# Optimization experiments

Measured on AMD Instinct MI355X. Metric: run time of the kernel, lower is better.

## Reference

```python
import jax, jax.numpy as jnp
import numpy as np

N_NODES = 50000
N_EDGES = 400000
IN_DIM = 64
HID = 128
HEADS = 4
NEG_SLOPE = 0.2


def gat_conv(x, src, dst, W, a_src, a_dst, b, heads, out_ch, concat):
    N = x.shape[0]
    h = (x @ W).reshape(N, heads, out_ch)                 # [N,H,C]
    alpha_s = jnp.einsum('nhc,hc->nh', h, a_src)          # [N,H]
    alpha_d = jnp.einsum('nhc,hc->nh', h, a_dst)
    e = jax.nn.leaky_relu(alpha_s[src] + alpha_d[dst], NEG_SLOPE)  # [E,H]
    m = jax.ops.segment_max(e, dst, num_segments=N)
    m = jnp.where(jnp.isfinite(m), m, 0.0)
    ex = jnp.exp(e - m[dst])
    s = jax.ops.segment_sum(ex, dst, num_segments=N)
    alpha = ex / s[dst]                                   # segment softmax over incoming edges
    out = jax.ops.segment_sum(h[src] * alpha[:, :, None], dst, num_segments=N)  # [N,H,C]
    out = out.reshape(N, heads * out_ch) if concat else out.mean(axis=1)
    return out + b


def setup_inputs() -> dict:
    key = jax.random.key(0)
    ks = jax.random.split(key, 20)
    g = lambda i, shape, sc: (jax.random.normal(ks[i], shape, jnp.float32) * sc)
    x = g(0, (N_NODES, IN_DIM), 1.0)
    edge_index = jax.random.randint(ks[1], (2, N_EDGES), 0, N_NODES, dtype=jnp.int32)
    d = {
        'x': x, 'edge_index': edge_index,
        'W1': g(2, (IN_DIM, HEADS * HID), 0.1), 'a_src1': g(3, (HEADS, HID), 0.1), 'a_dst1': g(4, (HEADS, HID), 0.1), 'b1': jnp.zeros((HEADS * HID,), jnp.float32),
        'W2': g(5, (HEADS * HID, HEADS * HID), 0.05), 'a_src2': g(6, (HEADS, HID), 0.1), 'a_dst2': g(7, (HEADS, HID), 0.1), 'b2': jnp.zeros((HEADS * HID,), jnp.float32),
        'W3': g(8, (HEADS * HID, HID), 0.05), 'a_src3': g(9, (1, HID), 0.1), 'a_dst3': g(10, (1, HID), 0.1), 'b3': jnp.zeros((HID,), jnp.float32),
        'fc1_w': g(11, (HID, HID // 2), 0.1), 'fc1_b': jnp.zeros((HID // 2,), jnp.float32),
        'fc2_w': g(12, (HID // 2, 1), 0.1), 'fc2_b': jnp.zeros((1,), jnp.float32),
    }
    return d


def reference(x, edge_index, W1, a_src1, a_dst1, b1, W2, a_src2, a_dst2, b2, W3, a_src3, a_dst3, b3, fc1_w, fc1_b, fc2_w, fc2_b):
    N = x.shape[0]
    loop = jnp.arange(N, dtype=edge_index.dtype)
    src = jnp.concatenate([edge_index[0], loop])  # PyG GATConv adds self-loops by default
    dst = jnp.concatenate([edge_index[1], loop])
    h = jax.nn.elu(gat_conv(x, src, dst, W1, a_src1, a_dst1, b1, HEADS, HID, True))
    h = jax.nn.elu(gat_conv(h, src, dst, W2, a_src2, a_dst2, b2, HEADS, HID, True))
    h = jax.nn.elu(gat_conv(h, src, dst, W3, a_src3, a_dst3, b3, 1, HID, False))
    h = jax.nn.relu(h @ fc1_w + fc1_b)
    return jax.nn.sigmoid(h @ fc2_w + fc2_b)  # [N, 1]
```

## Files before the change

### kernel.cpp

```cpp
#include <hip/hip_runtime.h>
#include <math.h>

typedef __attribute__((ext_vector_type(8))) short short8;
typedef __attribute__((ext_vector_type(4))) float f32x4;
typedef unsigned short u16;
typedef unsigned int u32;

__device__ inline u16 f2b(float f) {
  u32 u = __float_as_uint(f);
  return (u16)((u + 0x7FFFu + ((u >> 16) & 1u)) >> 16);
}
__device__ inline float b2f(u16 b) { return __uint_as_float((u32)b << 16); }
__device__ inline float lrelu(float v) { return v > 0.f ? v : 0.2f * v; }
__device__ inline float elu1(float v) { return v > 0.f ? v : __expf(v) - 1.f; }

__device__ inline void gld_lds16(const void* g, void* l) {
  __builtin_amdgcn_global_load_lds((const __attribute__((address_space(1))) void*)g,
                                   (__attribute__((address_space(3))) void*)l, 16, 0, 0);
}

__global__ void fused_prep(const float* __restrict__ W1, u16* __restrict__ Wt1,
                           const float* __restrict__ W2, u16* __restrict__ Wt2,
                           const float* __restrict__ W3, u16* __restrict__ Wt3,
                           const int* __restrict__ ei, int E0, int ET,
                           int* __restrict__ deg) {
  int i = blockIdx.x * blockDim.x + threadIdx.x;
  if (i < 64 * 512) {
    int k = i / 512, n = i % 512;
    Wt1[n * 64 + k] = f2b(W1[i]);
    return;
  }
  i -= 64 * 512;
  if (i < 512 * 512) {
    int k = i / 512, n = i % 512;
    Wt2[n * 512 + k] = f2b(W2[i]);
    return;
  }
  i -= 512 * 512;
  if (i < 512 * 128) {
    int k = i / 128, n = i % 128;
    Wt3[n * 512 + k] = f2b(W3[i]);
    return;
  }
  i -= 512 * 128;
  if (i < ET) {
    int d = (i < E0) ? ei[E0 + i] : (i - E0);
    atomicAdd(&deg[d], 1);
  }
}

__global__ __launch_bounds__(256) void gemm_bf16_gat(
    const u16* __restrict__ A, const u16* __restrict__ Bt, u16* __restrict__ Hb,
    const float* __restrict__ a_src, const float* __restrict__ a_dst,
    float* __restrict__ aS, float* __restrict__ aD, int M, int HC, int K, int Hh,
    int gy, int nStrips) {
  int mIdx, nIdx;
  if (nStrips == 4) {
    int l = blockIdx.x;
    int xcd = l & 7, k = l >> 3;
    nIdx = k & 3;
    mIdx = xcd + 8 * (k >> 2);
    if (mIdx >= gy) return;
  } else {
    mIdx = blockIdx.x;
    nIdx = 0;
  }
  __shared__ u16 As[2][128 * 32];
  __shared__ u16 Bs[2][128 * 32];
  __shared__ float sRed[2][2][128];
  const int tid = threadIdx.x;
  const int w = tid >> 6, lane = tid & 63;
  const int wm = w >> 1, wn = w & 1;
  const int q = lane >> 4, l15 = lane & 15;
  const int nBase = nIdx * 128;
  const int mBase = mIdx * 128;
  const int h = nBase >> 7;
  const int srow = lane >> 2;
  const int ssw = ((lane & 3) ^ ((lane >> 3) & 3)) * 8;
  const int rq = (q ^ ((l15 >> 1) & 3)) * 8;

  f32x4 acc[4][4];
#pragma unroll
  for (int i = 0; i < 4; ++i)
#pragma unroll
    for (int j = 0; j < 4; ++j) acc[i][j] = (f32x4){0.f, 0.f, 0.f, 0.f};

  const int nSteps = K >> 5;
#pragma unroll
  for (int r = 0; r < 2; ++r) {
    int lrow0 = w * 32 + r * 16;
    int ga = mBase + lrow0 + srow;
    if (ga >= M) ga = M - 1;
    gld_lds16(A + (size_t)ga * K + ssw, &As[0][lrow0 * 32]);
    int gb = nBase + lrow0 + srow;
    gld_lds16(Bt + (size_t)gb * K + ssw, &Bs[0][lrow0 * 32]);
  }
  __syncthreads();
  int cur = 0;
  for (int step = 0; step < nSteps; ++step) {
    const int k0n = (step + 1) << 5;
    if (k0n < K) {
#pragma unroll
      for (int r = 0; r < 2; ++r) {
        int lrow0 = w * 32 + r * 16;
        int ga = mBase + lrow0 + srow;
        if (ga >= M) ga = M - 1;
        gld_lds16(A + (size_t)ga * K + k0n + ssw, &As[cur ^ 1][lrow0 * 32]);
        int gb = nBase + lrow0 + srow;
        gld_lds16(Bt + (size_t)gb * K + k0n + ssw, &Bs[cur ^ 1][lrow0 * 32]);
      }
    }
    short8 af[4], bf[4];
#pragma unroll
    for (int i = 0; i < 4; ++i)
      af[i] = *(const short8*)&As[cur][(wm * 64 + i * 16 + l15) * 32 + rq];
#pragma unroll
    for (int j = 0; j < 4; ++j)
      bf[j] = *(const short8*)&Bs[cur][(wn * 64 + j * 16 + l15) * 32 + rq];
#pragma unroll
    for (int i = 0; i < 4; ++i)
#pragma unroll
      for (int j = 0; j < 4; ++j)
        acc[i][j] = __builtin_amdgcn_mfma_f32_16x16x32_bf16(af[i], bf[j], acc[i][j], 0, 0, 0);
    __syncthreads();
    cur ^= 1;
  }

  float asv[4], adv[4];
#pragma unroll
  for (int j = 0; j < 4; ++j) {
    int cw = wn * 64 + j * 16 + l15;
    asv[j] = a_src[h * 128 + cw];
    adv[j] = a_dst[h * 128 + cw];
  }
#pragma unroll
  for (int mi = 0; mi < 4; ++mi) {
#pragma unroll
    for (int r = 0; r < 4; ++r) {
      int row = mBase + wm * 64 + mi * 16 + q * 4 + r;
      float s = 0.f, d = 0.f;
#pragma unroll
      for (int j = 0; j < 4; ++j) {
        float v = acc[mi][j][r];
        s = fmaf(v, asv[j], s);
        d = fmaf(v, adv[j], d);
        if (row < M) Hb[(size_t)row * HC + nBase + wn * 64 + j * 16 + l15] = f2b(v);
      }
#pragma unroll
      for (int o = 8; o; o >>= 1) {
        s += __shfl_xor(s, o);
        d += __shfl_xor(d, o);
      }
      if (l15 == 0) {
        int lr = wm * 64 + mi * 16 + q * 4 + r;
        sRed[0][wn][lr] = s;
        sRed[1][wn][lr] = d;
      }
    }
  }
  __syncthreads();
  if (tid < 128) {
    int row = mBase + tid;
    if (row < M) {
      aS[(size_t)row * Hh + h] = sRed[0][0][tid] + sRed[0][1][tid];
      aD[(size_t)row * Hh + h] = sRed[1][0][tid] + sRed[1][1][tid];
    }
  }
}

__global__ __launch_bounds__(256) void gemm_bd_l1(
    const u16* __restrict__ A, const u16* __restrict__ Bt,
    const float* __restrict__ bias, u16* __restrict__ outB, int M, int gy) {
  int l = blockIdx.x;
  int xcd = l & 7, kk = l >> 3;
  int nIdx = kk & 3;
  int mIdx = xcd + 8 * (kk >> 2);
  if (mIdx >= gy) return;
  __shared__ u16 As[2][128 * 32];
  __shared__ u16 Bs[2][128 * 32];
  const int tid = threadIdx.x;
  const int w = tid >> 6, lane = tid & 63;
  const int wm = w >> 1, wn = w & 1;
  const int q = lane >> 4, l15 = lane & 15;
  const int nBase = nIdx * 128, mBase = mIdx * 128;
  const int srow = lane >> 2;
  const int ssw = ((lane & 3) ^ ((lane >> 3) & 3)) * 8;
  const int rq = (q ^ ((l15 >> 1) & 3)) * 8;

  f32x4 acc[4][4];
#pragma unroll
  for (int i = 0; i < 4; ++i)
#pragma unroll
    for (int j = 0; j < 4; ++j) acc[i][j] = (f32x4){0.f, 0.f, 0.f, 0.f};

#pragma unroll
  for (int r = 0; r < 2; ++r) {
    int lrow0 = w * 32 + r * 16;
    int ga = mBase + lrow0 + srow;
    if (ga >= M) ga = M - 1;
    gld_lds16(A + (size_t)ga * 256 + nIdx * 64 + ssw, &As[0][lrow0 * 32]);
    int gb = nBase + lrow0 + srow;
    gld_lds16(Bt + (size_t)gb * 64 + ssw, &Bs[0][lrow0 * 32]);
  }
  __syncthreads();
  int cur = 0;
#pragma unroll
  for (int step = 0; step < 2; ++step) {
    if (step == 0) {
#pragma unroll
      for (int r = 0; r < 2; ++r) {
        int lrow0 = w * 32 + r * 16;
        int ga = mBase + lrow0 + srow;
        if (ga >= M) ga = M - 1;
        gld_lds16(A + (size_t)ga * 256 + nIdx * 64 + 32 + ssw, &As[1][lrow0 * 32]);
        int gb = nBase + lrow0 + srow;
        gld_lds16(Bt + (size_t)gb * 64 + 32 + ssw, &Bs[1][lrow0 * 32]);
      }
    }
    short8 af[4], bf[4];
#pragma unroll
    for (int i = 0; i < 4; ++i)
      af[i] = *(const short8*)&As[cur][(wm * 64 + i * 16 + l15) * 32 + rq];
#pragma unroll
    for (int j = 0; j < 4; ++j)
      bf[j] = *(const short8*)&Bs[cur][(wn * 64 + j * 16 + l15) * 32 + rq];
#pragma unroll
    for (int i = 0; i < 4; ++i)
#pragma unroll
      for (int j = 0; j < 4; ++j)
        acc[i][j] = __builtin_amdgcn_mfma_f32_16x16x32_bf16(af[i], bf[j], acc[i][j], 0, 0, 0);
    __syncthreads();
    cur ^= 1;
  }

  float bvv[4];
#pragma unroll
  for (int j = 0; j < 4; ++j) bvv[j] = bias[nBase + wn * 64 + j * 16 + l15];
#pragma unroll
  for (int mi = 0; mi < 4; ++mi)
#pragma unroll
    for (int r = 0; r < 4; ++r) {
      int row = mBase + wm * 64 + mi * 16 + q * 4 + r;
      if (row < M) {
#pragma unroll
        for (int j = 0; j < 4; ++j) {
          float v = elu1(acc[mi][j][r] + bvv[j]);
          outB[(size_t)row * 512 + nBase + wn * 64 + j * 16 + l15] = f2b(v);
        }
      }
    }
}

__global__ __launch_bounds__(256) void scan_chunk(const int* __restrict__ deg,
                                                  int* __restrict__ incl,
                                                  int* __restrict__ bsums, int N) {
  __shared__ int sdata[256];
  const int t = threadIdx.x;
  const int base = blockIdx.x * 2048;
  int v[8];
  int sum = 0;
#pragma unroll
  for (int i = 0; i < 8; ++i) {
    int idx = base + t * 8 + i;
    v[i] = (idx < N) ? deg[idx] : 0;
    sum += v[i];
  }
  sdata[t] = sum;
  __syncthreads();
  for (int off = 1; off < 256; off <<= 1) {
    int x = (t >= off) ? sdata[t - off] : 0;
    __syncthreads();
    sdata[t] += x;
    __syncthreads();
  }
  int run = (t > 0) ? sdata[t - 1] : 0;
#pragma unroll
  for (int i = 0; i < 8; ++i) {
    int idx = base + t * 8 + i;
    run += v[i];
    if (idx < N) incl[idx] = run;
  }
  if (t == 255) bsums[blockIdx.x] = sdata[255];
}

__global__ void scan_final(const int* __restrict__ incl, const int* __restrict__ bsums,
                           int* __restrict__ rowptr, int N, int nb) {
  int i = blockIdx.x * blockDim.x + threadIdx.x;
  if (i >= N) return;
  int chunk = i >> 11;
  int pre = 0;
  for (int j = 0; j < chunk; ++j) pre += bsums[j];
  rowptr[i + 1] = incl[i] + pre;
  if (i == 0) rowptr[0] = 0;
}

__global__ void csr_fill(const int* __restrict__ ei, int E0, int ET,
                         const int* __restrict__ rowptr, int* __restrict__ cnt,
                         int* __restrict__ csr_src, int* __restrict__ csr_dst) {
  int e = blockIdx.x * blockDim.x + threadIdx.x;
  if (e >= ET) return;
  int s, d;
  if (e < E0) { s = ei[e]; d = ei[E0 + e]; }
  else        { s = e - E0; d = e - E0; }
  int pos = atomicAdd(&cnt[d], 1);
  csr_src[rowptr[d] + pos] = s;
  csr_dst[rowptr[d] + pos] = d;
}

__global__ void make_wsd(const float* __restrict__ W1, const float* __restrict__ as1,
                         const float* __restrict__ ad1, float* __restrict__ wsd) {
  int t = blockIdx.x * blockDim.x + threadIdx.x;
  if (t >= 512) return;
  int k = t >> 3, c8 = t & 7;
  int h = c8 & 3;
  const float* a = (c8 >= 4) ? ad1 : as1;
  float s = 0.f;
  for (int c = 0; c < 128; ++c) s += W1[k * 512 + h * 128 + c] * a[h * 128 + c];
  wsd[k * 8 + c8] = s;
}

__global__ __launch_bounds__(256) void asad_x(const float* __restrict__ xf,
                                              const float* __restrict__ wsd,
                                              float* __restrict__ aS,
                                              float* __restrict__ aD, int N) {
  const int wid = (int)((blockIdx.x * (blockDim.x >> 6)) + (threadIdx.x >> 6));
  const int lane = threadIdx.x & 63;
  if (wid >= N) return;
  float xv = xf[(size_t)wid * 64 + lane];
  float4 w0 = *(const float4*)&wsd[lane * 8];
  float4 w1 = *(const float4*)&wsd[lane * 8 + 4];
  float s[8] = {xv * w0.x, xv * w0.y, xv * w0.z, xv * w0.w,
                xv * w1.x, xv * w1.y, xv * w1.z, xv * w1.w};
#pragma unroll
  for (int i = 0; i < 8; ++i)
#pragma unroll
    for (int o = 32; o; o >>= 1) s[i] += __shfl_xor(s[i], o);
  if (lane == 0) {
    *(float4*)&aS[(size_t)wid * 4] = make_float4(s[0], s[1], s[2], s[3]);
    *(float4*)&aD[(size_t)wid * 4] = make_float4(s[4], s[5], s[6], s[7]);
  }
}

__global__ __launch_bounds__(256) void edge_logits(const int* __restrict__ csr_src,
                                                   const int* __restrict__ csr_dst,
                                                   const float* __restrict__ aS,
                                                   const float* __restrict__ aD,
                                                   float* __restrict__ elog, int ET,
                                                   int Hh) {
  int e = blockIdx.x * blockDim.x + threadIdx.x;
  if (e >= ET) return;
  int s = csr_src[e], d = csr_dst[e];
  if (Hh == 4) {
    float4 a = *(const float4*)&aS[(size_t)s * 4];
    float4 b = *(const float4*)&aD[(size_t)d * 4];
    float4 r;
    r.x = lrelu(a.x + b.x);
    r.y = lrelu(a.y + b.y);
    r.z = lrelu(a.z + b.z);
    r.w = lrelu(a.w + b.w);
    *(float4*)&elog[(size_t)e * 4] = r;
  } else {
    elog[e] = lrelu(aS[s] + aD[d]);
  }
}

__global__ __launch_bounds__(256) void gat_agg_x(
    const int* __restrict__ rowptr, const int* __restrict__ csr_src,
    const float* __restrict__ xf, const float* __restrict__ elog,
    u16* __restrict__ aggB, int N) {
  const int wid = (int)((blockIdx.x * (blockDim.x >> 6)) + (threadIdx.x >> 6));
  const int lane = threadIdx.x & 63;
  if (wid >= N) return;
  const int beg = rowptr[wid];
  const int deg = rowptr[wid + 1] - beg;
  const int h = lane >> 4;
  const int e16 = lane & 15;
  float acc[4] = {};

  if (deg <= 16) {
    int srcv = 0;
    float l = -1e30f;
    if (e16 < deg) {
      srcv = csr_src[beg + e16];
      l = elog[(size_t)(beg + e16) * 4 + h];
    }
    float xv[16];
#pragma unroll
    for (int j = 0; j < 16; ++j)
      if (j < deg) {
        int s = __shfl(srcv, j);
        xv[j] = xf[(size_t)s * 64 + lane];
      }
    float m = l;
#pragma unroll
    for (int o = 8; o; o >>= 1) m = fmaxf(m, __shfl_xor(m, o));
    float pexp = (e16 < deg) ? __expf(l - m) : 0.f;
    float cs = pexp;
#pragma unroll
    for (int o = 8; o; o >>= 1) cs += __shfl_xor(cs, o);
    pexp *= (1.f / cs);
#pragma unroll
    for (int j = 0; j < 16; ++j)
      if (j < deg) {
        float w0 = __shfl(pexp, j);
        float w1 = __shfl(pexp, 16 | j);
        float w2 = __shfl(pexp, 32 | j);
        float w3 = __shfl(pexp, 48 | j);
        acc[0] = fmaf(w0, xv[j], acc[0]);
        acc[1] = fmaf(w1, xv[j], acc[1]);
        acc[2] = fmaf(w2, xv[j], acc[2]);
        acc[3] = fmaf(w3, xv[j], acc[3]);
      }
  } else {
    float m = -1e30f, ssum = 0.f;
    for (int c = 0; c < deg; c += 16) {
      const int ce = min(16, deg - c);
      int srcv = 0;
      float l = -1e30f;
      if (e16 < ce) {
        srcv = csr_src[beg + c + e16];
        l = elog[(size_t)(beg + c + e16) * 4 + h];
      }
      float xv[16];
#pragma unroll
      for (int j = 0; j < 16; ++j)
        if (j < ce) {
          int s = __shfl(srcv, j);
          xv[j] = xf[(size_t)s * 64 + lane];
        }
      float cm = l;
#pragma unroll
      for (int o = 8; o; o >>= 1) cm = fmaxf(cm, __shfl_xor(cm, o));
      float pexp, cs;
      if (c == 0) {
        m = cm;
        pexp = (e16 < ce) ? __expf(l - m) : 0.f;
        cs = pexp;
#pragma unroll
        for (int o = 8; o; o >>= 1) cs += __shfl_xor(cs, o);
        ssum = cs;
      } else {
        float newm = fmaxf(m, cm);
        float r = __expf(m - newm);
        m = newm;
        pexp = (e16 < ce) ? __expf(l - m) : 0.f;
        cs = pexp;
#pragma unroll
        for (int o = 8; o; o >>= 1) cs += __shfl_xor(cs, o);
        ssum = ssum * r + cs;
#pragma unroll
        for (int i = 0; i < 4; ++i) acc[i] *= r;
      }
#pragma unroll
      for (int j = 0; j < 16; ++j)
        if (j < ce) {
          float w0 = __shfl(pexp, j);
          float w1 = __shfl(pexp, 16 | j);
          float w2 = __shfl(pexp, 32 | j);
          float w3 = __shfl(pexp, 48 | j);
          acc[0] = fmaf(w0, xv[j], acc[0]);
          acc[1] = fmaf(w1, xv[j], acc[1]);
          acc[2] = fmaf(w2, xv[j], acc[2]);
          acc[3] = fmaf(w3, xv[j], acc[3]);
        }
    }
    const float inv = 1.f / ssum;
#pragma unroll
    for (int i = 0; i < 4; ++i) acc[i] *= inv;
  }
#pragma unroll
  for (int hh = 0; hh < 4; ++hh)
    aggB[((size_t)wid * 4 + hh) * 64 + lane] = f2b(acc[hh]);
}

#define ACC8(A, pv, wgt)                                             \
  A[0] = fmaf(wgt, __uint_as_float(pv.x << 16), A[0]);               \
  A[1] = fmaf(wgt, __uint_as_float(pv.x & 0xffff0000u), A[1]);       \
  A[2] = fmaf(wgt, __uint_as_float(pv.y << 16), A[2]);               \
  A[3] = fmaf(wgt, __uint_as_float(pv.y & 0xffff0000u), A[3]);       \
  A[4] = fmaf(wgt, __uint_as_float(pv.z << 16), A[4]);               \
  A[5] = fmaf(wgt, __uint_as_float(pv.z & 0xffff0000u), A[5]);       \
  A[6] = fmaf(wgt, __uint_as_float(pv.w << 16), A[6]);               \
  A[7] = fmaf(wgt, __uint_as_float(pv.w & 0xffff0000u), A[7]);

__global__ __launch_bounds__(256) void gat_fused_agg(
    const int* __restrict__ rowptr, const int* __restrict__ csr_src,
    const u16* __restrict__ Hb, const float* __restrict__ elog,
    const float* __restrict__ bias, u16* __restrict__ outB,
    float* __restrict__ outF, int N) {
  const int wid = (int)((blockIdx.x * (blockDim.x >> 6)) + (threadIdx.x >> 6));
  const int lane = threadIdx.x & 63;
  if (wid >= N) return;
  const int beg = rowptr[wid];
  const int deg = rowptr[wid + 1] - beg;

  const int h = lane >> 4;
  const int e16 = lane & 15;
  const int c0 = lane * 8;
  const int hbase = lane & 48;
  float acc[8] = {};

  if (deg <= 16) {
    int srcv = 0;
    float l = -1e30f;
    if (e16 < deg) {
      srcv = csr_src[beg + e16];
      l = elog[(size_t)(beg + e16) * 4 + h];
    }
    uint4 pC[4];
#pragma unroll
    for (int j = 0; j < 4; ++j)
      if (j < deg) {
        int s = __shfl(srcv, j);
        pC[j] = *(const uint4*)&Hb[(size_t)s * 512 + c0];
      }
    float m = l;
#pragma unroll
    for (int o = 8; o; o >>= 1) m = fmaxf(m, __shfl_xor(m, o));
    float pexp = (e16 < deg) ? __expf(l - m) : 0.f;
    float cs = pexp;
#pragma unroll
    for (int o = 8; o; o >>= 1) cs += __shfl_xor(cs, o);
    pexp *= (1.f / cs);
    int e = 0;
    for (; e + 4 < deg; e += 4) {
      uint4 pN[4];
      int rem = deg - e - 4;
#pragma unroll
      for (int j = 0; j < 4; ++j)
        if (j < rem) {
          int s = __shfl(srcv, e + 4 + j);
          pN[j] = *(const uint4*)&Hb[(size_t)s * 512 + c0];
        }
#pragma unroll
      for (int j = 0; j < 4; ++j) {
        float wgt = __shfl(pexp, hbase | (e + j));
        ACC8(acc, pC[j], wgt)
      }
#pragma unroll
      for (int j = 0; j < 4; ++j) pC[j] = pN[j];
    }
#pragma unroll
    for (int j = 0; j < 4; ++j)
      if (j < deg - e) {
        float wgt = __shfl(pexp, hbase | (e + j));
        ACC8(acc, pC[j], wgt)
      }
  } else {
    float m = -1e30f, ssum = 0.f;
    for (int c = 0; c < deg; c += 16) {
      const int ce = min(16, deg - c);
      int srcv = 0;
      float l = -1e30f;
      if (e16 < ce) {
        srcv = csr_src[beg + c + e16];
        l = elog[(size_t)(beg + c + e16) * 4 + h];
      }
      float cm = l;
#pragma unroll
      for (int o = 8; o; o >>= 1) cm = fmaxf(cm, __shfl_xor(cm, o));
      float pexp, cs;
      if (c == 0) {
        m = cm;
        pexp = __expf(l - m);
        cs = pexp;
#pragma unroll
        for (int o = 8; o; o >>= 1) cs += __shfl_xor(cs, o);
        ssum = cs;
      } else {
        float newm = fmaxf(m, cm);
        float r = __expf(m - newm);
        m = newm;
        pexp = __expf(l - m);
        cs = pexp;
#pragma unroll
        for (int o = 8; o; o >>= 1) cs += __shfl_xor(cs, o);
        ssum = ssum * r + cs;
#pragma unroll
        for (int i = 0; i < 8; ++i) acc[i] *= r;
      }
      int e = 0;
      for (; e + 4 <= ce; e += 4) {
        int se0 = __shfl(srcv, e + 0), se1 = __shfl(srcv, e + 1);
        int se2 = __shfl(srcv, e + 2), se3 = __shfl(srcv, e + 3);
        float w0 = __shfl(pexp, hbase | (e + 0)), w1 = __shfl(pexp, hbase | (e + 1));
        float w2 = __shfl(pexp, hbase | (e + 2)), w3 = __shfl(pexp, hbase | (e + 3));
        uint4 p0 = *(const uint4*)&Hb[(size_t)se0 * 512 + c0];
        uint4 p1 = *(const uint4*)&Hb[(size_t)se1 * 512 + c0];
        uint4 p2 = *(const uint4*)&Hb[(size_t)se2 * 512 + c0];
        uint4 p3 = *(const uint4*)&Hb[(size_t)se3 * 512 + c0];
        ACC8(acc, p0, w0)
        ACC8(acc, p1, w1)
        ACC8(acc, p2, w2)
        ACC8(acc, p3, w3)
      }
      for (; e < ce; ++e) {
        int se = __shfl(srcv, e);
        float wgt = __shfl(pexp, hbase | e);
        uint4 pv = *(const uint4*)&Hb[(size_t)se * 512 + c0];
        ACC8(acc, pv, wgt)
      }
    }
    const float inv = 1.f / ssum;
#pragma unroll
    for (int i = 0; i < 8; ++i) acc[i] *= inv;
  }

  float bv[8];
  *(float4*)&bv[0] = *(const float4*)&bias[c0];
  *(float4*)&bv[4] = *(const float4*)&bias[c0 + 4];
  u16 packed[8];
#pragma unroll
  for (int i = 0; i < 8; ++i) {
    float v = elu1(acc[i] + bv[i]);
    acc[i] = v;
    packed[i] = f2b(v);
  }
  if (outB) *(uint4*)&outB[(size_t)wid * 512 + c0] = *(const uint4*)packed;
  if (outF) {
    *(float4*)&outF[(size_t)wid * 512 + c0] = make_float4(acc[0], acc[1], acc[2], acc[3]);
    *(float4*)&outF[(size_t)wid * 512 + c0 + 4] =
        make_float4(acc[4], acc[5], acc[6], acc[7]);
  }
}

__global__ __launch_bounds__(256) void gat_agg_h1(
    const int* __restrict__ rowptr, const int* __restrict__ csr_src,
    const u16* __restrict__ Hb, const float* __restrict__ elog,
    const float* __restrict__ bias, float* __restrict__ outF, int N) {
  const int wid = (int)((blockIdx.x * (blockDim.x >> 6)) + (threadIdx.x >> 6));
  const int lane = threadIdx.x & 63;
  if (wid >= N) return;
  const int beg = rowptr[wid];
  const int deg = rowptr[wid + 1] - beg;
  const int g = lane & 15;
  const int es = lane >> 4;
  const int c0 = g * 8;
  float acc[8] = {};

  if (deg <= 64) {
    int srcv = 0;
    float l = -1e30f;
    if (lane < deg) {
      srcv = csr_src[beg + lane];
      l = elog[beg + lane];
    }
    const int dm1 = deg - 1;
    uint4 pC;
    {
      int s = __shfl(srcv, min(es, dm1));
      pC = *(const uint4*)&Hb[(size_t)s * 128 + c0];
    }
    float m = l;
#pragma unroll
    for (int o = 32; o; o >>= 1) m = fmaxf(m, __shfl_xor(m, o));
    float pexp = (lane < deg) ? __expf(l - m) : 0.f;
    float cs = pexp;
#pragma unroll
    for (int o = 32; o; o >>= 1) cs += __shfl_xor(cs, o);
    pexp *= (1.f / cs);
    int t = 0;
    for (; t + 4 < deg; t += 4) {
      uint4 pN;
      {
        int s = __shfl(srcv, min(t + 4 + es, dm1));
        pN = *(const uint4*)&Hb[(size_t)s * 128 + c0];
      }
      float w = __shfl(pexp, t + es);
      ACC8(acc, pC, w)
      pC = pN;
    }
    {
      int idx = t + es;
      float w = __shfl(pexp, min(idx, dm1));
      if (idx > dm1) w = 0.f;
      ACC8(acc, pC, w)
    }
  } else {
    float m = -1e30f, ssum = 0.f;
    for (int c = 0; c < deg; c += 64) {
      const int ce = min(64, deg - c);
      int srcv = 0;
      float l = -1e30f;
      if (lane < ce) {
        srcv = csr_src[beg + c + lane];
        l = elog[beg + c + lane];
      }
      float cm = l;
#pragma unroll
      for (int o = 32; o; o >>= 1) cm = fmaxf(cm, __shfl_xor(cm, o));
      float pexp, cs;
      if (c == 0) {
        m = cm;
        pexp = __expf(l - m);
        cs = pexp;
#pragma unroll
        for (int o = 32; o; o >>= 1) cs += __shfl_xor(cs, o);
        ssum = cs;
      } else {
        float newm = fmaxf(m, cm);
        float r = __expf(m - newm);
        m = newm;
        pexp = __expf(l - m);
        cs = pexp;
#pragma unroll
        for (int o = 32; o; o >>= 1) cs += __shfl_xor(cs, o);
        ssum = ssum * r + cs;
#pragma unroll
        for (int i = 0; i < 8; ++i) acc[i] *= r;
      }
      for (int t = 0; t < ce; t += 4) {
        int idx = t + es;
        int se = __shfl(srcv, idx & 63);
        float wgt = __shfl(pexp, idx & 63);
        if (idx < ce) {
          uint4 pv = *(const uint4*)&Hb[(size_t)se * 128 + c0];
          ACC8(acc, pv, wgt)
        }
      }
    }
    const float inv = 1.f / ssum;
#pragma unroll
    for (int i = 0; i < 8; ++i) acc[i] *= inv;
  }
#pragma unroll
  for (int i = 0; i < 8; ++i) {
    acc[i] += __shfl_xor(acc[i], 16);
    acc[i] += __shfl_xor(acc[i], 32);
  }
  if (lane < 16) {
    float o[8];
#pragma unroll
    for (int i = 0; i < 8; ++i) o[i] = elu1(acc[i] + bias[c0 + i]);
    *(float4*)&outF[(size_t)wid * 128 + c0] = make_float4(o[0], o[1], o[2], o[3]);
    *(float4*)&outF[(size_t)wid * 128 + c0 + 4] = make_float4(o[4], o[5], o[6], o[7]);
  }
}

__global__ __launch_bounds__(256) void fc_head(const float* __restrict__ A,
                                               const float* __restrict__ B,
                                               const float* __restrict__ bias,
                                               const float* __restrict__ w2,
                                               const float* __restrict__ b2,
                                               float* __restrict__ out, int M) {
  __shared__ float As[16][64];
  __shared__ float Bs[16][64];
  __shared__ float sP[64][17];
  const int tid = threadIdx.x;
  const int tx = tid & 15, ty = tid >> 4;
  const int mBase = blockIdx.y * 64;
  const int aRow = tid >> 2;
  const int aK = (tid & 3) << 2;
  const int bC = tid & 63;
  const int bR0 = tid >> 6;
  const int K = 128, N = 64;
  float acc[4][4] = {};
  for (int k0 = 0; k0 < K; k0 += 16) {
    float4 av = make_float4(0.f, 0.f, 0.f, 0.f);
    int gr = mBase + aRow;
    if (gr < M) av = *(const float4*)&A[(size_t)gr * K + k0 + aK];
    As[aK + 0][aRow] = av.x;
    As[aK + 1][aRow] = av.y;
    As[aK + 2][aRow] = av.z;
    As[aK + 3][aRow] = av.w;
#pragma unroll
    for (int i = 0; i < 4; ++i) {
      int r = bR0 + i * 4;
      Bs[r][bC] = B[(size_t)(k0 + r) * N + bC];
    }
    __syncthreads();
#pragma unroll
    for (int k = 0; k < 16; ++k) {
      float4 a = *(const float4*)&As[k][ty * 4];
      float4 b = *(const float4*)&Bs[k][tx * 4];
      float ar[4] = {a.x, a.y, a.z, a.w};
      float br[4] = {b.x, b.y, b.z, b.w};
#pragma unroll
      for (int i = 0; i < 4; ++i)
#pragma unroll
        for (int j = 0; j < 4; ++j) acc[i][j] = fmaf(ar[i], br[j], acc[i][j]);
    }
    __syncthreads();
  }
  float4 bv = *(const float4*)&bias[tx * 4];
  float4 wv = *(const float4*)&w2[tx * 4];
#pragma unroll
  for (int i = 0; i < 4; ++i) {
    float p = 0.f;
    p = fmaf(fmaxf(acc[i][0] + bv.x, 0.f), wv.x, p);
    p = fmaf(fmaxf(acc[i][1] + bv.y, 0.f), wv.y, p);
    p = fmaf(fmaxf(acc[i][2] + bv.z, 0.f), wv.z, p);
    p = fmaf(fmaxf(acc[i][3] + bv.w, 0.f), wv.w, p);
    sP[ty * 4 + i][tx] = p;
  }
  __syncthreads();
  if (tid < 64) {
    int row = mBase + tid;
    if (row < M) {
      float s = 0.f;
#pragma unroll
      for (int t = 0; t < 16; ++t) s += sP[tid][t];
      out[row] = 1.f / (1.f + expf(-(s + b2[0])));
    }
  }
}

extern "C" void kernel_launch(void* const* d_in, const int* in_sizes, int n_in,
                              void* d_out, int out_size, void* d_ws, size_t ws_size,
                              hipStream_t stream) {
  const float* x    = (const float*)d_in[0];
  const int*   ei   = (const int*)d_in[1];
  const float* W1   = (const float*)d_in[2];
  const float* as1  = (const float*)d_in[3];
  const float* ad1  = (const float*)d_in[4];
  const float* b1   = (const float*)d_in[5];
  const float* W2   = (const float*)d_in[6];
  const float* as2  = (const float*)d_in[7];
  const float* ad2  = (const float*)d_in[8];
  const float* b2   = (const float*)d_in[9];
  const float* W3   = (const float*)d_in[10];
  const float* as3  = (const float*)d_in[11];
  const float* ad3  = (const float*)d_in[12];
  const float* b3   = (const float*)d_in[13];
  const float* fc1w = (const float*)d_in[14];
  const float* fc1b = (const float*)d_in[15];
  const float* fc2w = (const float*)d_in[16];
  const float* fc2b = (const float*)d_in[17];
  float* out = (float*)d_out;

  const int N  = in_sizes[0] / 64;
  const int E0 = in_sizes[1] / 2;
  const int ET = E0 + N;

  char* ws = (char*)d_ws;
  size_t off = 0;
  auto alloc = [&](size_t bytes) -> void* {
    void* p = ws + off;
    off += (bytes + 255) & ~(size_t)255;
    return p;
  };
  u16*   bufXb   = (u16*)alloc((size_t)N * 512 * 2);
  u16*   bufHb   = (u16*)alloc((size_t)N * 512 * 2);
  float* bufF    = (float*)alloc((size_t)N * 128 * 4);
  float* aS      = (float*)alloc((size_t)N * 4 * 4);
  float* aD      = (float*)alloc((size_t)N * 4 * 4);
  u16*   Wt1     = (u16*)alloc((size_t)512 * 64 * 2);
  u16*   Wt2     = (u16*)alloc((size_t)512 * 512 * 2);
  u16*   Wt3     = (u16*)alloc((size_t)128 * 512 * 2);
  u16*   aggB    = (u16*)alloc((size_t)N * 256 * 2);
  float* wsd     = (float*)alloc((size_t)64 * 8 * 4);
  int*   degcnt  = (int*)alloc((size_t)2 * N * 4);
  int*   deg     = degcnt;
  int*   cnt     = degcnt + N;
  int*   incl    = (int*)alloc((size_t)N * 4);
  int*   rowptr  = (int*)alloc((size_t)(N + 1) * 4);
  int*   bsums   = (int*)alloc(256 * 4);
  int*   csr_src = (int*)alloc((size_t)ET * 4);
  int*   csr_dst = (int*)alloc((size_t)ET * 4);
  float* elog    = (float*)alloc((size_t)ET * 4 * 4);
  (void)ws_size; (void)n_in; (void)out_size;

  hipMemsetAsync(degcnt, 0, (size_t)2 * N * 4, stream);
  const int prepTotal = 64 * 512 + 512 * 512 + 512 * 128 + ET;
  hipLaunchKernelGGL(fused_prep, dim3((prepTotal + 255) / 256), dim3(256), 0, stream,
                     W1, Wt1, W2, Wt2, W3, Wt3, ei, E0, ET, deg);

  int nb = (N + 2047) / 2048;
  hipLaunchKernelGGL(scan_chunk, dim3(nb), dim3(256), 0, stream, deg, incl, bsums, N);
  hipLaunchKernelGGL(scan_final, dim3((N + 255) / 256), dim3(256), 0, stream, incl, bsums,
                     rowptr, N, nb);
  int eb = (ET + 255) / 256;
  hipLaunchKernelGGL(csr_fill, dim3(eb), dim3(256), 0, stream, ei, E0, ET, rowptr, cnt,
                     csr_src, csr_dst);

  const int gy = (N + 127) / 128;
  const int grid4 = ((gy + 7) / 8) * 8 * 4;
  const int aggGrid = (N + 3) / 4;

  hipLaunchKernelGGL(make_wsd, dim3(2), dim3(256), 0, stream, W1, as1, ad1, wsd);
  hipLaunchKernelGGL(asad_x, dim3(aggGrid), dim3(256), 0, stream, x, wsd, aS, aD, N);
  hipLaunchKernelGGL(edge_logits, dim3(eb), dim3(256), 0, stream, csr_src, csr_dst, aS,
                     aD, elog, ET, 4);
  hipLaunchKernelGGL(gat_agg_x, dim3(aggGrid), dim3(256), 0, stream, rowptr, csr_src, x,
                     elog, aggB, N);
  hipLaunchKernelGGL(gemm_bd_l1, dim3(grid4), dim3(256), 0, stream, aggB, Wt1, b1,
                     bufXb, N, gy);

  hipLaunchKernelGGL(gemm_bf16_gat, dim3(grid4), dim3(256), 0, stream, bufXb, Wt2, bufHb,
                     as2, ad2, aS, aD, N, 512, 512, 4, gy, 4);
  hipLaunchKernelGGL(edge_logits, dim3(eb), dim3(256), 0, stream, csr_src, csr_dst, aS,
                     aD, elog, ET, 4);
  hipLaunchKernelGGL(gat_fused_agg, dim3(aggGrid), dim3(256), 0, stream, rowptr,
                     csr_src, bufHb, elog, b2, bufXb, nullptr, N);

  hipLaunchKernelGGL(gemm_bf16_gat, dim3(gy), dim3(256), 0, stream, bufXb, Wt3, bufHb,
                     as3, ad3, aS, aD, N, 128, 512, 1, gy, 1);
  hipLaunchKernelGGL(edge_logits, dim3(eb), dim3(256), 0, stream, csr_src, csr_dst, aS,
                     aD, elog, ET, 1);
  hipLaunchKernelGGL(gat_agg_h1, dim3(aggGrid), dim3(256), 0, stream, rowptr, csr_src,
                     bufHb, elog, b3, bufF, N);

  hipLaunchKernelGGL(fc_head, dim3(1, (N + 63) / 64), dim3(256), 0, stream, bufF, fc1w,
                     fc1b, fc2w, fc2b, out, N);
}
```

Before: 451.2 us.

## Split-K layer-3 GEMM, halve-width layer-2 aggregation, fold wsd into prep

Layer 3's GEMM (N=128 output, single strip) now runs as a split-K kernel over two K halves, writing fp32 partials that a new reduce kernel sums, converts to bf16 and uses to compute attention logits. The layer-2 aggregation assigns two waves per node, each covering half the 512 channels with 8-byte loads, which doubles parallelism and lowers per-wave register use. The small make_wsd launch is folded into fused_prep. The split-K path adds an extra fp32 partial write and read pass plus one more kernel launch.

```diff
diff --git a/kernel.cpp b/kernel.cpp
--- a/kernel.cpp
+++ b/kernel.cpp
@@ -23,7 +23,8 @@
                            const float* __restrict__ W2, u16* __restrict__ Wt2,
                            const float* __restrict__ W3, u16* __restrict__ Wt3,
                            const int* __restrict__ ei, int E0, int ET,
-                           int* __restrict__ deg) {
+                           int* __restrict__ deg, const float* __restrict__ as1,
+                           const float* __restrict__ ad1, float* __restrict__ wsd) {
   int i = blockIdx.x * blockDim.x + threadIdx.x;
   if (i < 64 * 512) {
     int k = i / 512, n = i % 512;
@@ -46,6 +47,15 @@
   if (i < ET) {
     int d = (i < E0) ? ei[E0 + i] : (i - E0);
     atomicAdd(&deg[d], 1);
+    return;
+  }
+  i -= ET;
+  if (i < 512) {
+    int k = i >> 3, c8 = i & 7, hh = c8 & 3;
+    const float* a = (c8 >= 4) ? ad1 : as1;
+    float s = 0.f;
+    for (int c = 0; c < 128; ++c) s += W1[k * 512 + hh * 128 + c] * a[hh * 128 + c];
+    wsd[k * 8 + c8] = s;
   }
 }
 
@@ -165,6 +175,111 @@
       aS[(size_t)row * Hh + h] = sRed[0][0][tid] + sRed[0][1][tid];
       aD[(size_t)row * Hh + h] = sRed[1][0][tid] + sRed[1][1][tid];
     }
+  }
+}
+
+__global__ __launch_bounds__(256) void gemm_bf16_l3(
+    const u16* __restrict__ A, const u16* __restrict__ Bt, float* __restrict__ p0,
+    float* __restrict__ p1, int M, int gy) {
+  int b = blockIdx.x;
+  int kh = (b >= gy) ? 1 : 0;
+  int mIdx = b - kh * gy;
+  float* __restrict__ P = kh ? p1 : p0;
+  const int kOff = kh * 256;
+  __shared__ u16 As[2][128 * 32];
+  __shared__ u16 Bs[2][128 * 32];
+  const int tid = threadIdx.x;
+  const int w = tid >> 6, lane = tid & 63;
+  const int wm = w >> 1, wn = w & 1;
+  const int q = lane >> 4, l15 = lane & 15;
+  const int mBase = mIdx * 128;
+  const int srow = lane >> 2;
+  const int ssw = ((lane & 3) ^ ((lane >> 3) & 3)) * 8;
+  const int rq = (q ^ ((l15 >> 1) & 3)) * 8;
+
+  f32x4 acc[4][4];
+#pragma unroll
+  for (int i = 0; i < 4; ++i)
+#pragma unroll
+    for (int j = 0; j < 4; ++j) acc[i][j] = (f32x4){0.f, 0.f, 0.f, 0.f};
+
+#pragma unroll
+  for (int r = 0; r < 2; ++r) {
+    int lrow0 = w * 32 + r * 16;
+    int ga = mBase + lrow0 + srow;
+    if (ga >= M) ga = M - 1;
+    gld_lds16(A + (size_t)ga * 512 + kOff + ssw, &As[0][lrow0 * 32]);
+    int gb = lrow0 + srow;
+    gld_lds16(Bt + (size_t)gb * 512 + kOff + ssw, &Bs[0][lrow0 * 32]);
+  }
+  __syncthreads();
+  int cur = 0;
+  for (int step = 0; step < 8; ++step) {
+    if (step < 7) {
+      const int k0n = kOff + ((step + 1) << 5);
+#pragma unroll
+      for (int r = 0; r < 2; ++r) {
+        int lrow0 = w * 32 + r * 16;
+        int ga = mBase + lrow0 + srow;
+        if (ga >= M) ga = M - 1;
+        gld_lds16(A + (size_t)ga * 512 + k0n + ssw, &As[cur ^ 1][lrow0 * 32]);
+        int gb = lrow0 + srow;
+        gld_lds16(Bt + (size_t)gb * 512 + k0n + ssw, &Bs[cur ^ 1][lrow0 * 32]);
+      }
+    }
+    short8 af[4], bf[4];
+#pragma unroll
+    for (int i = 0; i < 4; ++i)
+      af[i] = *(const short8*)&As[cur][(wm * 64 + i * 16 + l15) * 32 + rq];
+#pragma unroll
+    for (int j = 0; j < 4; ++j)
+      bf[j] = *(const short8*)&Bs[cur][(wn * 64 + j * 16 + l15) * 32 + rq];
+#pragma unroll
+    for (int i = 0; i < 4; ++i)
+#pragma unroll
+      for (int j = 0; j < 4; ++j)
+        acc[i][j] = __builtin_amdgcn_mfma_f32_16x16x32_bf16(af[i], bf[j], acc[i][j], 0, 0, 0);
+    __syncthreads();
+    cur ^= 1;
+  }
+#pragma unroll
+  for (int mi = 0; mi < 4; ++mi)
+#pragma unroll
+    for (int r = 0; r < 4; ++r) {
+      int row = mBase + wm * 64 + mi * 16 + q * 4 + r;
+      if (row < M) {
+#pragma unroll
+        for (int j = 0; j < 4; ++j)
+          P[(size_t)row * 128 + wn * 64 + j * 16 + l15] = acc[mi][j][r];
+      }
+    }
+}
+
+__global__ __launch_bounds__(256) void l3_reduce(
+    const float* __restrict__ p0, const float* __restrict__ p1,
+    const float* __restrict__ a_src, const float* __restrict__ a_dst,
+    u16* __restrict__ Hb, float* __restrict__ aS, float* __restrict__ aD, int N) {
+  const int wid = (int)((blockIdx.x * (blockDim.x >> 6)) + (threadIdx.x >> 6));
+  const int lane = threadIdx.x & 63;
+  if (wid >= N) return;
+  const int c2 = lane * 2;
+  float2 u0 = *(const float2*)&p0[(size_t)wid * 128 + c2];
+  float2 u1 = *(const float2*)&p1[(size_t)wid * 128 + c2];
+  float v0 = u0.x + u1.x, v1 = u0.y + u1.y;
+  u32 pk = (u32)f2b(v0) | ((u32)f2b(v1) << 16);
+  *(u32*)&Hb[(size_t)wid * 128 + c2] = pk;
+  float2 asv = *(const float2*)&a_src[c2];
+  float2 adv = *(const float2*)&a_dst[c2];
+  float s = v0 * asv.x + v1 * asv.y;
+  float d = v0 * adv.x + v1 * adv.y;
+#pragma unroll
+  for (int o = 32; o; o >>= 1) {
+    s += __shfl_xor(s, o);
+    d += __shfl_xor(d, o);
+  }
+  if (lane == 0) {
+    aS[wid] = s;
+    aD[wid] = d;
   }
 }
 
@@ -305,18 +420,6 @@
   int pos = atomicAdd(&cnt[d], 1);
   csr_src[rowptr[d] + pos] = s;
   csr_dst[rowptr[d] + pos] = d;
-}
-
-__global__ void make_wsd(const float* __restrict__ W1, const float* __restrict__ as1,
-                         const float* __restrict__ ad1, float* __restrict__ wsd) {
-  int t = blockIdx.x * blockDim.x + threadIdx.x;
-  if (t >= 512) return;
-  int k = t >> 3, c8 = t & 7;
-  int h = c8 & 3;
-  const float* a = (c8 >= 4) ? ad1 : as1;
-  float s = 0.f;
-  for (int c = 0; c < 128; ++c) s += W1[k * 512 + h * 128 + c] * a[h * 128 + c];
-  wsd[k * 8 + c8] = s;
 }
 
 __global__ __launch_bounds__(256) void asad_x(const float* __restrict__ xf,
@@ -473,6 +576,12 @@
     aggB[((size_t)wid * 4 + hh) * 64 + lane] = f2b(acc[hh]);
 }
 
+#define ACC4(A, pv, wgt)                                             \
+  A[0] = fmaf(wgt, __uint_as_float(pv.x << 16), A[0]);               \
+  A[1] = fmaf(wgt, __uint_as_float(pv.x & 0xffff0000u), A[1]);       \
+  A[2] = fmaf(wgt, __uint_as_float(pv.y << 16), A[2]);               \
+  A[3] = fmaf(wgt, __uint_as_float(pv.y & 0xffff0000u), A[3]);
+
 #define ACC8(A, pv, wgt)                                             \
   A[0] = fmaf(wgt, __uint_as_float(pv.x << 16), A[0]);               \
   A[1] = fmaf(wgt, __uint_as_float(pv.x & 0xffff0000u), A[1]);       \
@@ -486,19 +595,19 @@
 __global__ __launch_bounds__(256) void gat_fused_agg(
     const int* __restrict__ rowptr, const int* __restrict__ csr_src,
     const u16* __restrict__ Hb, const float* __restrict__ elog,
-    const float* __restrict__ bias, u16* __restrict__ outB,
-    float* __restrict__ outF, int N) {
-  const int wid = (int)((blockIdx.x * (blockDim.x >> 6)) + (threadIdx.x >> 6));
+    const float* __restrict__ bias, u16* __restrict__ outB, int N) {
+  const int wgl = (int)((blockIdx.x * (blockDim.x >> 6)) + (threadIdx.x >> 6));
+  if (wgl >= 2 * N) return;
+  const int wid = wgl >> 1, half = wgl & 1;
   const int lane = threadIdx.x & 63;
-  if (wid >= N) return;
   const int beg = rowptr[wid];
   const int deg = rowptr[wid + 1] - beg;
 
   const int h = lane >> 4;
   const int e16 = lane & 15;
-  const int c0 = lane * 8;
-  const int hbase = lane & 48;
-  float acc[8] = {};
+  const int c0 = half * 256 + lane * 4;
+  const int hbase = (((half << 1) | (lane >> 5)) << 4);
+  float acc[4] = {};
 
   if (deg <= 16) {
     int srcv = 0;
@@ -507,12 +616,12 @@
       srcv = csr_src[beg + e16];
       l = elog[(size_t)(beg + e16) * 4 + h];
     }
-    uint4 pC[4];
+    uint2 pC[4];
 #pragma unroll
     for (int j = 0; j < 4; ++j)
       if (j < deg) {
         int s = __shfl(srcv, j);
-        pC[j] = *(const uint4*)&Hb[(size_t)s * 512 + c0];
+        pC[j] = *(const uint2*)&Hb[(size_t)s * 512 + c0];
       }
     float m = l;
 #pragma unroll
@@ -524,18 +633,18 @@
     pexp *= (1.f / cs);
     int e = 0;
     for (; e + 4 < deg; e += 4) {
-      uint4 pN[4];
+      uint2 pN[4];
       int rem = deg - e - 4;
 #pragma unroll
       for (int j = 0; j < 4; ++j)
         if (j < rem) {
           int s = __shfl(srcv, e + 4 + j);
-          pN[j] = *(const uint4*)&Hb[(size_t)s * 512 + c0];
+          pN[j] = *(const uint2*)&Hb[(size_t)s * 512 + c0];
         }
 #pragma unroll
       for (int j = 0; j < 4; ++j) {
         float wgt = __shfl(pexp, hbase | (e + j));
-        ACC8(acc, pC[j], wgt)
+        ACC4(acc, pC[j], wgt)
       }
 #pragma unroll
       for (int j = 0; j < 4; ++j) pC[j] = pN[j];
@@ -544,7 +653,7 @@
     for (int j = 0; j < 4; ++j)
       if (j < deg - e) {
         float wgt = __shfl(pexp, hbase | (e + j));
-        ACC8(acc, pC[j], wgt)
+        ACC4(acc, pC[j], wgt)
       }
   } else {
     float m = -1e30f, ssum = 0.f;
@@ -577,7 +686,7 @@
         for (int o = 8; o; o >>= 1) cs += __shfl_xor(cs, o);
         ssum = ssum * r + cs;
 #pragma unroll
-        for (int i = 0; i < 8; ++i) acc[i] *= r;
+        for (int i = 0; i < 4; ++i) acc[i] *= r;
       }
       int e = 0;
       for (; e + 4 <= ce; e += 4) {
@@ -585,43 +694,36 @@
         int se2 = __shfl(srcv, e + 2), se3 = __shfl(srcv, e + 3);
         float w0 = __shfl(pexp, hbase | (e + 0)), w1 = __shfl(pexp, hbase | (e + 1));
         float w2 = __shfl(pexp, hbase | (e + 2)), w3 = __shfl(pexp, hbase | (e + 3));
-        uint4 p0 = *(const uint4*)&Hb[(size_t)se0 * 512 + c0];
-        uint4 p1 = *(const uint4*)&Hb[(size_t)se1 * 512 + c0];
-        uint4 p2 = *(const uint4*)&Hb[(size_t)se2 * 512 + c0];
-        uint4 p3 = *(const uint4*)&Hb[(size_t)se3 * 512 + c0];
-        ACC8(acc, p0, w0)
-        ACC8(acc, p1, w1)
-        ACC8(acc, p2, w2)
-        ACC8(acc, p3, w3)
+        uint2 p0 = *(const uint2*)&Hb[(size_t)se0 * 512 + c0];
+        uint2 p1 = *(const uint2*)&Hb[(size_t)se1 * 512 + c0];
+        uint2 p2 = *(const uint2*)&Hb[(size_t)se2 * 512 + c0];
+        uint2 p3 = *(const uint2*)&Hb[(size_t)se3 * 512 + c0];
+        ACC4(acc, p0, w0)
+        ACC4(acc, p1, w1)
+        ACC4(acc, p2, w2)
+        ACC4(acc, p3, w3)
       }
       for (; e < ce; ++e) {
         int se = __shfl(srcv, e);
         float wgt = __shfl(pexp, hbase | e);
-        uint4 pv = *(const uint4*)&Hb[(size_t)se * 512 + c0];
-        ACC8(acc, pv, wgt)
+        uint2 pv = *(const uint2*)&Hb[(size_t)se * 512 + c0];
+        ACC4(acc, pv, wgt)
       }
     }
     const float inv = 1.f / ssum;
 #pragma unroll
-    for (int i = 0; i < 8; ++i) acc[i] *= inv;
-  }
-
-  float bv[8];
-  *(float4*)&bv[0] = *(const float4*)&bias[c0];
-  *(float4*)&bv[4] = *(const float4*)&bias[c0 + 4];
-  u16 packed[8];
-#pragma unroll
-  for (int i = 0; i < 8; ++i) {
-    float v = elu1(acc[i] + bv[i]);
-    acc[i] = v;
-    packed[i] = f2b(v);
-  }
-  if (outB) *(uint4*)&outB[(size_t)wid * 512 + c0] = *(const uint4*)packed;
-  if (outF) {
-    *(float4*)&outF[(size_t)wid * 512 + c0] = make_float4(acc[0], acc[1], acc[2], acc[3]);
-    *(float4*)&outF[(size_t)wid * 512 + c0 + 4] =
-        make_float4(acc[4], acc[5], acc[6], acc[7]);
-  }
+    for (int i = 0; i < 4; ++i) acc[i] *= inv;
+  }
+
+  float4 bv = *(const float4*)&bias[c0];
+  u16 k0 = f2b(elu1(acc[0] + bv.x));
+  u16 k1 = f2b(elu1(acc[1] + bv.y));
+  u16 k2 = f2b(elu1(acc[2] + bv.z));
+  u16 k3 = f2b(elu1(acc[3] + bv.w));
+  uint2 o;
+  o.x = (u32)k0 | ((u32)k1 << 16);
+  o.y = (u32)k2 | ((u32)k3 << 16);
+  *(uint2*)&outB[(size_t)wid * 512 + c0] = o;
 }
 
 __global__ __launch_bounds__(256) void gat_agg_h1(
@@ -845,7 +947,7 @@
   float* aS      = (float*)alloc((size_t)N * 4 * 4);
   float* aD      = (float*)alloc((size_t)N * 4 * 4);
   u16*   Wt1     = (u16*)alloc((size_t)512 * 64 * 2);
-  u16*   Wt2     = (u16*)alloc((size_t)512 * 512 * 2);
+  u16*   Wt2    = (u16*)alloc((size_t)512 * 512 * 2);
   u16*   Wt3     = (u16*)alloc((size_t)128 * 512 * 2);
   u16*   aggB    = (u16*)alloc((size_t)N * 256 * 2);
   float* wsd     = (float*)alloc((size_t)64 * 8 * 4);
@@ -861,9 +963,9 @@
   (void)ws_size; (void)n_in; (void)out_size;
 
   hipMemsetAsync(degcnt, 0, (size_t)2 * N * 4, stream);
-  const int prepTotal = 64 * 512 + 512 * 512 + 512 * 128 + ET;
+  const int prepTotal = 64 * 512 + 512 * 512 + 512 * 128 + ET + 512;
   hipLaunchKernelGGL(fused_prep, dim3((prepTotal + 255) / 256), dim3(256), 0, stream,
-                     W1, Wt1, W2, Wt2, W3, Wt3, ei, E0, ET, deg);
+                     W1, Wt1, W2, Wt2, W3, Wt3, ei, E0, ET, deg, as1, ad1, wsd);
 
   int nb = (N + 2047) / 2048;
   hipLaunchKernelGGL(scan_chunk, dim3(nb), dim3(256), 0, stream, deg, incl, bsums, N);
@@ -876,8 +978,8 @@
   const int gy = (N + 127) / 128;
   const int grid4 = ((gy + 7) / 8) * 8 * 4;
   const int aggGrid = (N + 3) / 4;
-
-  hipLaunchKernelGGL(make_wsd, dim3(2), dim3(256), 0, stream, W1, as1, ad1, wsd);
+  const int aggGrid2 = (2 * N + 3) / 4;
+
   hipLaunchKernelGGL(asad_x, dim3(aggGrid), dim3(256), 0, stream, x, wsd, aS, aD, N);
   hipLaunchKernelGGL(edge_logits, dim3(eb), dim3(256), 0, stream, csr_src, csr_dst, aS,
                      aD, elog, ET, 4);
@@ -890,11 +992,13 @@
                      as2, ad2, aS, aD, N, 512, 512, 4, gy, 4);
   hipLaunchKernelGGL(edge_logits, dim3(eb), dim3(256), 0, stream, csr_src, csr_dst, aS,
                      aD, elog, ET, 4);
-  hipLaunchKernelGGL(gat_fused_agg, dim3(aggGrid), dim3(256), 0, stream, rowptr,
-                     csr_src, bufHb, elog, b2, bufXb, nullptr, N);
-
-  hipLaunchKernelGGL(gemm_bf16_gat, dim3(gy), dim3(256), 0, stream, bufXb, Wt3, bufHb,
-                     as3, ad3, aS, aD, N, 128, 512, 1, gy, 1);
+  hipLaunchKernelGGL(gat_fused_agg, dim3(aggGrid2), dim3(256), 0, stream, rowptr,
+                     csr_src, bufHb, elog, b2, bufXb, N);
+
+  hipLaunchKernelGGL(gemm_bf16_l3, dim3(2 * gy), dim3(256), 0, stream, bufXb, Wt3,
+                     bufF, (float*)aggB, N, gy);
+  hipLaunchKernelGGL(l3_reduce, dim3(aggGrid), dim3(256), 0, stream, (const float*)bufF,
+                     (const float*)aggB, as3, ad3, bufHb, aS, aD, N);
   hipLaunchKernelGGL(edge_logits, dim3(eb), dim3(256), 0, stream, csr_src, csr_dst, aS,
                      aD, elog, ET, 1);
   hipLaunchKernelGGL(gat_agg_h1, dim3(aggGrid), dim3(256), 0, stream, rowptr, csr_src,
```

Result: slower. 468.2 us (+3.8%).
